# Performance work log

Hardware: AMD Instinct MI355X
Metric: run time of the kernel (lower is better)

## Reference

```python
import jax, jax.numpy as jnp
import numpy as np

N, D, R, B, K = 16384, 300, 10, 1024, 64


def setup_inputs() -> dict:
    key = jax.random.key(0)
    ks = jax.random.split(key, 6)
    return {
        "node_feat_src": jax.random.normal(ks[0], (N, D), jnp.float32),
        "node_feat_tgt": jax.random.normal(ks[1], (N, D), jnp.float32),
        "srcs_index": jax.random.randint(ks[2], (B, K), 0, N),
        "tgts_index": jax.random.randint(ks[3], (B, K), 0, N),
        "src_vs": jax.random.normal(ks[4], (R, D), jnp.float32),
        "tgt_vs": jax.random.normal(ks[5], (R, D), jnp.float32),
    }


def _tower(h, vs):
    # Householder chain: h @ (I - v v^T / (v^T v)) == h - ((h v) / (v^T v)) v^T
    def step(h, v):
        coef = (h @ v) / (v @ v)  # [N]
        return h - coef[:, None] * v[None, :], None
    h, _ = jax.lax.scan(step, h, vs)
    return h


def _l2norm(x):
    # matches F.normalize(p=2, eps=1e-12) over the last dim
    n = jnp.linalg.norm(x, axis=-1, keepdims=True)
    return x / jnp.maximum(n, 1e-12)


def reference(node_feat_src, node_feat_tgt, srcs_index, tgts_index, src_vs, tgt_vs):
    src_h = _tower(node_feat_src, src_vs)  # [N, D]
    tgt_h = _tower(node_feat_tgt, tgt_vs)  # [N, D]

    pos_src = _l2norm(src_h[srcs_index[:, 0]])  # [B, D]
    pos_tgt = _l2norm(tgt_h[tgts_index[:, 0]])  # [B, D]
    src_list = _l2norm(src_h[srcs_index])       # [B, K, D]
    tgt_list = _l2norm(tgt_h[tgts_index])       # [B, K, D]

    sim_src2tgt = jnp.einsum('bd,bkd->bk', pos_src, tgt_list)  # [B, K]
    sim_tgt2src = jnp.einsum('bd,bkd->bk', pos_tgt, src_list)  # [B, K]

    # CSLS hubness penalties: mean of top-10 cross-domain cosine sims
    sim_matrix = _l2norm(src_h) @ _l2norm(tgt_h).T  # [N, N]
    rt = jnp.mean(jax.lax.top_k(sim_matrix, 10)[0], axis=1)    # [N]
    rs = jnp.mean(jax.lax.top_k(sim_matrix.T, 10)[0], axis=1)  # [N]

    srcs_rt = rt[srcs_index]  # [B, K]
    tgts_rs = rs[tgts_index]  # [B, K]

    logits_src2tgt = sim_src2tgt * 2 - srcs_rt[:, 0:1] - tgts_rs
    logits_tgt2src = sim_tgt2src * 2 - tgts_rs[:, 0:1] - srcs_rt
    return logits_src2tgt, logits_tgt2src
```

## Files before the change

kernel.cpp:

```cpp
#include <hip/hip_runtime.h>
#include <hip/hip_bf16.h>

#define NN 16384
#define DD 300
#define DP 320
#define RR 10
#define BB 1024
#define KK 64
#define CAP 128
#define CAPL 512

typedef __attribute__((ext_vector_type(8))) short s8v;
typedef __attribute__((ext_vector_type(4))) float f4v;
typedef _Float16 h2 __attribute__((ext_vector_type(2)));

__device__ __forceinline__ unsigned mono2(unsigned d) {
    unsigned s = ((d >> 15) & 0x10001u) * 0xFFFFu;
    return d ^ (s | 0x80008000u);
}
__device__ __forceinline__ float key2f16(unsigned k) {
    unsigned short b = (k & 0x8000u) ? (unsigned short)(k ^ 0x8000u)
                                     : (unsigned short)(~k & 0xFFFFu);
    _Float16 hv = __builtin_bit_cast(_Float16, b);
    return (float)hv;
}

__device__ __forceinline__ h2 h2max(h2 a, h2 b) {
    return __builtin_elementwise_max(a, b);
}
__device__ __forceinline__ h2 hmax2s(h2 a, int xb) {
    int x = __shfl_xor(__builtin_bit_cast(int, a), xb);
    return h2max(a, __builtin_bit_cast(h2, x));
}
__device__ __forceinline__ h2 packh2(float a, float b) {
    h2 r; r[0] = (_Float16)a; r[1] = (_Float16)b; return r;
}

__device__ __forceinline__ void ins10(unsigned (&lst)[10], unsigned v) {
    #pragma unroll
    for (int q = 0; q < 10; ++q) {
        unsigned a  = lst[q];
        unsigned mx = a > v ? a : v;
        v           = a > v ? v : a;
        lst[q] = mx;
    }
}
__device__ __forceinline__ void ins10f(float (&lst)[10], float v) {
    #pragma unroll
    for (int q = 0; q < 10; ++q) {
        float a  = lst[q];
        float mx = fmaxf(a, v);
        v        = fminf(a, v);
        lst[q] = mx;
    }
}

__device__ __forceinline__ void xcd_map(int bid, int& by, int& bx) {
    const int xcd = bid & 7;
    const int s   = bid >> 3;
    bx = (xcd << 2) | (s & 3);
    by = s >> 2;
}

__device__ __forceinline__ void gload_lds16(const void* g, void* l) {
#if __has_builtin(__builtin_amdgcn_global_load_lds)
    __builtin_amdgcn_global_load_lds(
        (const __attribute__((address_space(1))) void*)g,
        (__attribute__((address_space(3))) void*)l, 16, 0, 0);
#else
    const int lane = threadIdx.x & 63;
    int4 v = *reinterpret_cast<const int4*>(g);
    *reinterpret_cast<int4*>((char*)l + lane * 16) = v;
#endif
}

__device__ __forceinline__ void stage_tile(
        const __hip_bfloat16* __restrict__ Ab, const __hip_bfloat16* __restrict__ Bb,
        int kb, char* base, int w, int lane) {
    const int r8 = lane >> 3;
    const int u  = (lane & 7) ^ r8;
    const int row = w * 8 + r8;
    const size_t go = (size_t)row * DP + kb * 64 + u * 8;
    gload_lds16(Ab + go, base + w * 1024);
    gload_lds16(Bb + go, base + 16384 + w * 1024);
}

__global__ __launch_bounds__(256) void tower_kernel(
        const float* __restrict__ feat, const float* __restrict__ vs,
        __hip_bfloat16* __restrict__ out) {
    __shared__ float vsh[RR * DD];
    const int tid = threadIdx.x;
    for (int i = tid; i < RR * DD; i += 256) vsh[i] = vs[i];
    __syncthreads();

    const int lane = tid & 63;
    const int wave = tid >> 6;
    const int row  = blockIdx.x * 4 + wave;

    float h[5];
    #pragma unroll
    for (int j = 0; j < 5; ++j) {
        int d = lane + 64 * j;
        h[j] = (d < DD) ? feat[(size_t)row * DD + d] : 0.f;
    }
    #pragma unroll
    for (int r = 0; r < RR; ++r) {
        float vl[5];
        float hv = 0.f, vv = 0.f;
        #pragma unroll
        for (int j = 0; j < 5; ++j) {
            int d = lane + 64 * j;
            float v = (d < DD) ? vsh[r * DD + d] : 0.f;
            vl[j] = v;
            hv += h[j] * v;
            vv += v * v;
        }
        #pragma unroll
        for (int o = 32; o; o >>= 1) {
            hv += __shfl_xor(hv, o);
            vv += __shfl_xor(vv, o);
        }
        float coef = hv / vv;
        #pragma unroll
        for (int j = 0; j < 5; ++j) h[j] -= coef * vl[j];
    }
    float nn = 0.f;
    #pragma unroll
    for (int j = 0; j < 5; ++j) nn += h[j] * h[j];
    #pragma unroll
    for (int o = 32; o; o >>= 1) nn += __shfl_xor(nn, o);
    float scale = 1.f / fmaxf(sqrtf(nn), 1e-12f);
    #pragma unroll
    for (int j = 0; j < 5; ++j) {
        int d = lane + 64 * j;
        float val = (d < DD) ? h[j] * scale : 0.f;
        out[(size_t)row * DP + d] = __float2bfloat16(val);
    }
}

#define KLOOP(COMPUTE_BODY)                                                    \
    stage_tile(Ab, Bb, 0, u_lds, w, lane);                                     \
    _Pragma("unroll")                                                          \
    for (int kb = 0; kb < 5; ++kb) {                                           \
        char* curb = u_lds + (kb & 1) * 32768;                                 \
        if (kb < 4)                                                            \
            stage_tile(Ab, Bb, kb + 1, u_lds + ((kb + 1) & 1) * 32768, w, lane); \
        if (kb < 4) { asm volatile("s_waitcnt vmcnt(2)" ::: "memory"); }       \
        else        { asm volatile("s_waitcnt vmcnt(0)" ::: "memory"); }       \
        __builtin_amdgcn_s_barrier();                                          \
        asm volatile("" ::: "memory");                                         \
        {                                                                      \
            const __hip_bfloat16* Asub = (const __hip_bfloat16*)curb;          \
            const __hip_bfloat16* Bsub = (const __hip_bfloat16*)(curb + 16384);\
            COMPUTE_BODY                                                       \
        }                                                                      \
        asm volatile("" ::: "memory");                                         \
        __builtin_amdgcn_s_barrier();                                          \
    }

#define COMPUTE_TILE                                                           \
    _Pragma("unroll")                                                          \
    for (int ks = 0; ks < 2; ++ks) {                                           \
        s8v af[2], bfv[2];                                                     \
        const int ulog = ks * 4 + (lane >> 4);                                 \
        const int up   = ulog ^ (lane & 7);                                    \
        _Pragma("unroll")                                                      \
        for (int m = 0; m < 2; ++m) {                                          \
            const int row = wr * 32 + m * 16 + (lane & 15);                    \
            af[m] = *reinterpret_cast<const s8v*>(Asub + row * 64 + up * 8);   \
        }                                                                      \
        _Pragma("unroll")                                                      \
        for (int n = 0; n < 2; ++n) {                                          \
            const int row = wc * 32 + n * 16 + (lane & 15);                    \
            bfv[n] = *reinterpret_cast<const s8v*>(Bsub + row * 64 + up * 8);  \
        }                                                                      \
        _Pragma("unroll")                                                      \
        for (int m = 0; m < 2; ++m)                                            \
            _Pragma("unroll")                                                  \
            for (int n = 0; n < 2; ++n)                                        \
                acc[m][n] = __builtin_amdgcn_mfma_f32_16x16x32_bf16(           \
                    af[m], bfv[n], acc[m][n], 0, 0, 0);                        \
    }

__global__ __launch_bounds__(1024) void passA_kernel(
        const __hip_bfloat16* __restrict__ A, const __hip_bfloat16* __restrict__ Bm,
        unsigned short* __restrict__ rowsmax_g,
        unsigned short* __restrict__ colsmax_g) {
    __shared__ __align__(16) char u_lds[65536];
    __shared__ unsigned short rowsm[16][512];
    __shared__ unsigned short colsm[512][16];

    const int tid = threadIdx.x;
    const int lane = tid & 63;
    const int w = tid >> 6;
    const int wr = w >> 2, wc = w & 3;
    int by, bx; xcd_map(blockIdx.x, by, bx);
    const int i0 = by * 512, j0 = bx * 512;

    for (int ti = 0; ti < 4; ++ti) {
        for (int tj = 0; tj < 4; ++tj) {
            f4v acc[2][2];
            #pragma unroll
            for (int m = 0; m < 2; ++m)
                #pragma unroll
                for (int n = 0; n < 2; ++n)
                    acc[m][n] = (f4v){0.f, 0.f, 0.f, 0.f};

            const __hip_bfloat16* Ab = A  + (size_t)(i0 + ti * 128) * DP;
            const __hip_bfloat16* Bb = Bm + (size_t)(j0 + tj * 128) * DP;

            KLOOP(COMPUTE_TILE)

            #pragma unroll
            for (int m = 0; m < 2; ++m) {
                h2 a01 = h2max(packh2(acc[m][0][0], acc[m][0][1]),
                               packh2(acc[m][1][0], acc[m][1][1]));
                h2 a23 = h2max(packh2(acc[m][0][2], acc[m][0][3]),
                               packh2(acc[m][1][2], acc[m][1][3]));
                a01 = hmax2s(a01, 1); a23 = hmax2s(a23, 1);
                a01 = hmax2s(a01, 2); a23 = hmax2s(a23, 2);
                a01 = hmax2s(a01, 4); a23 = hmax2s(a23, 4);
                a01 = hmax2s(a01, 8); a23 = hmax2s(a23, 8);
                if ((lane & 15) == m * 8) {
                    const int rl = ti * 128 + wr * 32 + m * 16 + ((lane >> 4) << 2);
                    uint2 u = make_uint2(mono2(__builtin_bit_cast(unsigned, a01)),
                                         mono2(__builtin_bit_cast(unsigned, a23)));
                    *reinterpret_cast<uint2*>(&rowsm[tj * 4 + wc][rl]) = u;
                }
            }
            {
                float rm0 = -1e30f, rm1 = -1e30f;
                #pragma unroll
                for (int m = 0; m < 2; ++m) {
                    rm0 = fmaxf(rm0, fmaxf(fmaxf(acc[m][0][0], acc[m][0][1]),
                                           fmaxf(acc[m][0][2], acc[m][0][3])));
                    rm1 = fmaxf(rm1, fmaxf(fmaxf(acc[m][1][0], acc[m][1][1]),
                                           fmaxf(acc[m][1][2], acc[m][1][3])));
                }
                h2 c = packh2(rm0, rm1);
                c = hmax2s(c, 16);
                c = hmax2s(c, 32);
                if ((lane >> 4) == 0) {
                    const int s = ti * 4 + wr;
                    const int cb = tj * 128 + wc * 32 + (lane & 15);
                    unsigned k = mono2(__builtin_bit_cast(unsigned, c));
                    colsm[cb][s]      = (unsigned short)(k & 0xFFFFu);
                    colsm[cb + 16][s] = (unsigned short)(k >> 16);
                }
            }
        }
    }
    __syncthreads();
    if (tid < 512) {
        const int r = tid;
        unsigned short t16[16];
        #pragma unroll
        for (int s = 0; s < 16; ++s) t16[s] = rowsm[s][r];
        uint4 o0, o1;
        o0.x = t16[0] | ((unsigned)t16[1] << 16);  o0.y = t16[2] | ((unsigned)t16[3] << 16);
        o0.z = t16[4] | ((unsigned)t16[5] << 16);  o0.w = t16[6] | ((unsigned)t16[7] << 16);
        o1.x = t16[8] | ((unsigned)t16[9] << 16);  o1.y = t16[10] | ((unsigned)t16[11] << 16);
        o1.z = t16[12] | ((unsigned)t16[13] << 16); o1.w = t16[14] | ((unsigned)t16[15] << 16);
        uint4* rdst = reinterpret_cast<uint4*>(rowsmax_g + (size_t)(i0 + r) * 512 + bx * 16);
        rdst[0] = o0; rdst[1] = o1;
    } else {
        const int r = tid - 512;
        uint4 q0 = *reinterpret_cast<uint4*>(&colsm[r][0]);
        uint4 q1 = *reinterpret_cast<uint4*>(&colsm[r][8]);
        uint4* cdst = reinterpret_cast<uint4*>(colsmax_g + (size_t)(j0 + r) * 512 + by * 16);
        cdst[0] = q0; cdst[1] = q1;
    }
}

__global__ __launch_bounds__(256) void thresh_kernel(
        const unsigned short* __restrict__ rowsmax_g,
        const unsigned short* __restrict__ colsmax_g,
        float* __restrict__ Tlb_row, float* __restrict__ Tlb_col,
        unsigned* __restrict__ rowcnt, unsigned* __restrict__ colcnt) {
    const int t = blockIdx.x * 256 + threadIdx.x;
    const bool isRow = t < NN;
    const int idx = isRow ? t : t - NN;
    const unsigned short* src = (isRow ? rowsmax_g : colsmax_g) + (size_t)idx * 512;

    unsigned lst[10];
    #pragma unroll
    for (int q = 0; q < 10; ++q) lst[q] = 0u;

    const uint4* p = reinterpret_cast<const uint4*>(src);
    for (int c = 0; c < 64; ++c) {
        uint4 q = p[c];
        unsigned v0 = q.x & 0xFFFFu, v1 = q.x >> 16;
        unsigned v2 = q.y & 0xFFFFu, v3 = q.y >> 16;
        unsigned v4 = q.z & 0xFFFFu, v5 = q.z >> 16;
        unsigned v6 = q.w & 0xFFFFu, v7 = q.w >> 16;
        unsigned g01 = v0 > v1 ? v0 : v1, g23 = v2 > v3 ? v2 : v3;
        unsigned g45 = v4 > v5 ? v4 : v5, g67 = v6 > v7 ? v6 : v7;
        unsigned ga = g01 > g23 ? g01 : g23, gb = g45 > g67 ? g45 : g67;
        unsigned g = ga > gb ? ga : gb;
        if (g > lst[9]) {
            if (v0 > lst[9]) ins10(lst, v0);
            if (v1 > lst[9]) ins10(lst, v1);
            if (v2 > lst[9]) ins10(lst, v2);
            if (v3 > lst[9]) ins10(lst, v3);
            if (v4 > lst[9]) ins10(lst, v4);
            if (v5 > lst[9]) ins10(lst, v5);
            if (v6 > lst[9]) ins10(lst, v6);
            if (v7 > lst[9]) ins10(lst, v7);
        }
    }
    float f = key2f16(lst[9]);
    float lb = f - fabsf(f) * 0.002f - 1e-6f;
    if (isRow) { Tlb_row[idx] = lb; rowcnt[idx] = 0u; }
    else       { Tlb_col[idx] = lb; colcnt[idx] = 0u; }
}

__global__ __launch_bounds__(1024) void passB_kernel(
        const __hip_bfloat16* __restrict__ A, const __hip_bfloat16* __restrict__ Bm,
        const float* __restrict__ Tlb_row, const float* __restrict__ Tlb_col,
        unsigned* __restrict__ rowcnt, unsigned* __restrict__ colcnt,
        float* __restrict__ rowbuf, float* __restrict__ colbuf) {
    __shared__ __align__(16) char u_lds[65536];
    __shared__ float Trow_s[512];
    __shared__ float Tcol_s[512];
    __shared__ unsigned scnt[2];
    __shared__ uint2 sbuf[2][CAPL];

    const int tid = threadIdx.x;
    const int lane = tid & 63;
    const int w = tid >> 6;
    const int wr = w >> 2, wc = w & 3;
    int by, bx; xcd_map(blockIdx.x, by, bx);
    const int i0 = by * 512, j0 = bx * 512;

    if (tid < 512) Trow_s[tid] = Tlb_row[i0 + tid];
    else           Tcol_s[tid - 512] = Tlb_col[j0 + tid - 512];
    if (tid < 2) scnt[tid] = 0u;
    __syncthreads();

    for (int ti = 0; ti < 4; ++ti) {
        float trmin = 1e30f;
        #pragma unroll
        for (int m = 0; m < 2; ++m)
            #pragma unroll
            for (int r = 0; r < 4; ++r)
                trmin = fminf(trmin, Trow_s[ti * 128 + wr * 32 + m * 16 + ((lane >> 4) << 2) + r]);

        for (int tj = 0; tj < 4; ++tj) {
            f4v acc[2][2];
            #pragma unroll
            for (int m = 0; m < 2; ++m)
                #pragma unroll
                for (int n = 0; n < 2; ++n)
                    acc[m][n] = (f4v){0.f, 0.f, 0.f, 0.f};

            const __hip_bfloat16* Ab = A  + (size_t)(i0 + ti * 128) * DP;
            const __hip_bfloat16* Bb = Bm + (size_t)(j0 + tj * 128) * DP;

            KLOOP(COMPUTE_TILE)

            const int c0i = tj * 128 + wc * 32 + (lane & 15);
            const int c1i = c0i + 16;
            const float tc0 = Tcol_s[c0i], tc1 = Tcol_s[c1i];
            float vm = -1e30f;
            #pragma unroll
            for (int m = 0; m < 2; ++m) {
                float a = fmaxf(fmaxf(acc[m][0][0], acc[m][0][1]),
                                fmaxf(acc[m][0][2], acc[m][0][3]));
                float b = fmaxf(fmaxf(acc[m][1][0], acc[m][1][1]),
                                fmaxf(acc[m][1][2], acc[m][1][3]));
                vm = fmaxf(vm, fmaxf(a, b));
            }
            if (vm >= fminf(trmin, fminf(tc0, tc1))) {
                #pragma unroll
                for (int m = 0; m < 2; ++m) {
                    #pragma unroll
                    for (int r = 0; r < 4; ++r) {
                        const int rl = ti * 128 + wr * 32 + m * 16 + ((lane >> 4) << 2) + r;
                        const float T = Trow_s[rl];
                        const float v0 = acc[m][0][r], v1 = acc[m][1][r];
                        if (v0 >= T) {
                            unsigned p = atomicAdd(&scnt[0], 1u);
                            if (p < CAPL) sbuf[0][p] = make_uint2((unsigned)(i0 + rl), __float_as_uint(v0));
                            else { unsigned q = atomicAdd(&rowcnt[i0 + rl], 1u);
                                   if (q < CAP) rowbuf[(size_t)(i0 + rl) * CAP + q] = v0; }
                        }
                        if (v1 >= T) {
                            unsigned p = atomicAdd(&scnt[0], 1u);
                            if (p < CAPL) sbuf[0][p] = make_uint2((unsigned)(i0 + rl), __float_as_uint(v1));
                            else { unsigned q = atomicAdd(&rowcnt[i0 + rl], 1u);
                                   if (q < CAP) rowbuf[(size_t)(i0 + rl) * CAP + q] = v1; }
                        }
                        if (v0 >= tc0) {
                            unsigned p = atomicAdd(&scnt[1], 1u);
                            if (p < CAPL) sbuf[1][p] = make_uint2((unsigned)(j0 + c0i), __float_as_uint(v0));
                            else { unsigned q = atomicAdd(&colcnt[j0 + c0i], 1u);
                                   if (q < CAP) colbuf[(size_t)(j0 + c0i) * CAP + q] = v0; }
                        }
                        if (v1 >= tc1) {
                            unsigned p = atomicAdd(&scnt[1], 1u);
                            if (p < CAPL) sbuf[1][p] = make_uint2((unsigned)(j0 + c1i), __float_as_uint(v1));
                            else { unsigned q = atomicAdd(&colcnt[j0 + c1i], 1u);
                                   if (q < CAP) colbuf[(size_t)(j0 + c1i) * CAP + q] = v1; }
                        }
                    }
                }
            }
        }
    }

    __syncthreads();
    {
        const unsigned nr = scnt[0] < CAPL ? scnt[0] : CAPL;
        const unsigned nc = scnt[1] < CAPL ? scnt[1] : CAPL;
        for (unsigned i = tid; i < nr; i += 1024) {
            uint2 e = sbuf[0][i];
            unsigned p = atomicAdd(&rowcnt[e.x], 1u);
            if (p < CAP) rowbuf[(size_t)e.x * CAP + p] = __uint_as_float(e.y);
        }
        for (unsigned i = tid; i < nc; i += 1024) {
            uint2 e = sbuf[1][i];
            unsigned p = atomicAdd(&colcnt[e.x], 1u);
            if (p < CAP) colbuf[(size_t)e.x * CAP + p] = __uint_as_float(e.y);
        }
    }
}

__global__ __launch_bounds__(256) void final_kernel(
        const unsigned* __restrict__ rowcnt, const unsigned* __restrict__ colcnt,
        const float* __restrict__ rowbuf, const float* __restrict__ colbuf,
        float* __restrict__ rt, float* __restrict__ rs) {
    const int t = blockIdx.x * 256 + threadIdx.x;
    const bool isRow = t < NN;
    const int idx = isRow ? t : t - NN;
    const unsigned cn = (isRow ? rowcnt : colcnt)[idx];
    const int n = (int)(cn < CAP ? cn : CAP);
    const float* buf = (isRow ? rowbuf : colbuf) + (size_t)idx * CAP;

    float lst[10];
    #pragma unroll
    for (int q = 0; q < 10; ++q) lst[q] = -1e30f;
    for (int i = 0; i < n; ++i) {
        float v = buf[i];
        if (v > lst[9]) ins10f(lst, v);
    }
    float s = 0.f;
    #pragma unroll
    for (int q = 0; q < 10; ++q) s += lst[q];
    s *= 0.1f;
    (isRow ? rt : rs)[idx] = s;
}

__global__ __launch_bounds__(256) void logits_kernel(
        const __hip_bfloat16* __restrict__ srcH, const __hip_bfloat16* __restrict__ tgtH,
        const int* __restrict__ sidx, const int* __restrict__ tidx,
        const float* __restrict__ rt, const float* __restrict__ rs,
        float* __restrict__ out) {
    const int b    = blockIdx.x;
    const int lane = threadIdx.x & 63;
    const int w    = threadIdx.x >> 6;

    const int s0 = sidx[b * KK];
    const int t0 = tidx[b * KK];
    float ps[5], pt[5];
    #pragma unroll
    for (int j = 0; j < 5; ++j) {
        int d = lane + 64 * j;
        ps[j] = __bfloat162float(srcH[(size_t)s0 * DP + d]);
        pt[j] = __bfloat162float(tgtH[(size_t)t0 * DP + d]);
    }
    const float rt_s0 = rt[s0];
    const float rs_t0 = rs[t0];

    for (int kk = w; kk < KK; kk += 4) {
        const int it = tidx[b * KK + kk];
        const int is = sidx[b * KK + kk];
        float a = 0.f, c = 0.f;
        #pragma unroll
        for (int j = 0; j < 5; ++j) {
            int d = lane + 64 * j;
            a += ps[j] * __bfloat162float(tgtH[(size_t)it * DP + d]);
            c += pt[j] * __bfloat162float(srcH[(size_t)is * DP + d]);
        }
        #pragma unroll
        for (int o = 32; o; o >>= 1) {
            a += __shfl_xor(a, o);
            c += __shfl_xor(c, o);
        }
        if (lane == 0) {
            out[b * KK + kk]           = 2.f * a - rt_s0 - rs[it];
            out[BB * KK + b * KK + kk] = 2.f * c - rs_t0 - rt[is];
        }
    }
}

extern "C" void kernel_launch(void* const* d_in, const int* in_sizes, int n_in,
                              void* d_out, int out_size, void* d_ws, size_t ws_size,
                              hipStream_t stream) {
    const float* nf_src = (const float*)d_in[0];
    const float* nf_tgt = (const float*)d_in[1];
    const int*   sidx   = (const int*)d_in[2];
    const int*   tidx   = (const int*)d_in[3];
    const float* svs    = (const float*)d_in[4];
    const float* tvs    = (const float*)d_in[5];

    char* ws = (char*)d_ws;
    const size_t SZ_H  = (size_t)NN * DP * 2;
    const size_t SZ_SM = (size_t)NN * 512 * 2;
    __hip_bfloat16* srcH = (__hip_bfloat16*)ws;
    __hip_bfloat16* tgtH = (__hip_bfloat16*)(ws + SZ_H);
    unsigned short* rowsmax = (unsigned short*)(ws + 2 * SZ_H);
    unsigned short* colsmax = (unsigned short*)(ws + 2 * SZ_H + SZ_SM);
    float* rowbuf = (float*)(ws + 2 * SZ_H);
    float* colbuf = (float*)(ws + 2 * SZ_H + (size_t)NN * CAP * 4);
    char* tail = ws + 2 * SZ_H + 2 * SZ_SM;
    float* Tlb_row = (float*)(tail);
    float* Tlb_col = (float*)(tail + 65536);
    unsigned* rowcnt = (unsigned*)(tail + 2 * 65536);
    unsigned* colcnt = (unsigned*)(tail + 3 * 65536);
    float* rt = (float*)(tail + 4 * 65536);
    float* rs = (float*)(tail + 5 * 65536);

    tower_kernel<<<NN / 4, 256, 0, stream>>>(nf_src, svs, srcH);
    tower_kernel<<<NN / 4, 256, 0, stream>>>(nf_tgt, tvs, tgtH);
    passA_kernel<<<1024, 1024, 0, stream>>>(srcH, tgtH, rowsmax, colsmax);
    thresh_kernel<<<(2 * NN) / 256, 256, 0, stream>>>(rowsmax, colsmax, Tlb_row, Tlb_col,
                                                      rowcnt, colcnt);
    passB_kernel<<<1024, 1024, 0, stream>>>(srcH, tgtH, Tlb_row, Tlb_col,
                                            rowcnt, colcnt, rowbuf, colbuf);
    final_kernel<<<(2 * NN) / 256, 256, 0, stream>>>(rowcnt, colcnt, rowbuf, colbuf, rt, rs);
    logits_kernel<<<BB, 256, 0, stream>>>(srcH, tgtH, sidx, tidx, rt, rs, (float*)d_out);
}
```

Baseline: 632.8 us.

## Use 256-thread blocks with 64x64 per-wave MFMA tiles in GEMM passes

Both GEMM passes now run 4 waves per block instead of 16, and each wave computes a 64x64 sub-tile (4x4 MFMA accumulators) instead of 32x32. This raises register-level reuse of the LDS fragments and cuts LDS read traffic per MFMA. In exchange the double-buffered async prefetch is replaced by a single buffer with syncthreads around each stage, so global loads no longer overlap compute inside a block. The max-reduction and threshold-scan epilogues are reworked to match the new accumulator layout.

```diff
diff --git a/kernel.cpp b/kernel.cpp
--- a/kernel.cpp
+++ b/kernel.cpp
@@ -34,6 +34,9 @@
 }
 __device__ __forceinline__ h2 packh2(float a, float b) {
     h2 r; r[0] = (_Float16)a; r[1] = (_Float16)b; return r;
+}
+__device__ __forceinline__ float max4(f4v v) {
+    return fmaxf(fmaxf(v[0], v[1]), fmaxf(v[2], v[3]));
 }
 
 __device__ __forceinline__ void ins10(unsigned (&lst)[10], unsigned v) {
@@ -79,10 +82,15 @@
         int kb, char* base, int w, int lane) {
     const int r8 = lane >> 3;
     const int u  = (lane & 7) ^ r8;
-    const int row = w * 8 + r8;
-    const size_t go = (size_t)row * DP + kb * 64 + u * 8;
-    gload_lds16(Ab + go, base + w * 1024);
-    gload_lds16(Bb + go, base + 16384 + w * 1024);
+    #pragma unroll
+    for (int qq = 0; qq < 8; ++qq) {
+        const int chunk = qq * 4 + w;
+        const int cm = chunk & 15;
+        const int row = cm * 8 + r8;
+        const size_t go = (size_t)row * DP + kb * 64 + u * 8;
+        gload_lds16((chunk < 16 ? Ab : Bb) + go,
+                    base + (chunk < 16 ? 0 : 16384) + cm * 1024);
+    }
 }
 
 __global__ __launch_bounds__(256) void tower_kernel(
@@ -138,121 +146,110 @@
     }
 }
 
-#define KLOOP(COMPUTE_BODY)                                                    \
-    stage_tile(Ab, Bb, 0, u_lds, w, lane);                                     \
+#define KLOOP64                                                                \
     _Pragma("unroll")                                                          \
     for (int kb = 0; kb < 5; ++kb) {                                           \
-        char* curb = u_lds + (kb & 1) * 32768;                                 \
-        if (kb < 4)                                                            \
-            stage_tile(Ab, Bb, kb + 1, u_lds + ((kb + 1) & 1) * 32768, w, lane); \
-        if (kb < 4) { asm volatile("s_waitcnt vmcnt(2)" ::: "memory"); }       \
-        else        { asm volatile("s_waitcnt vmcnt(0)" ::: "memory"); }       \
-        __builtin_amdgcn_s_barrier();                                          \
-        asm volatile("" ::: "memory");                                         \
-        {                                                                      \
-            const __hip_bfloat16* Asub = (const __hip_bfloat16*)curb;          \
-            const __hip_bfloat16* Bsub = (const __hip_bfloat16*)(curb + 16384);\
-            COMPUTE_BODY                                                       \
+        __syncthreads();                                                       \
+        stage_tile(Ab, Bb, kb, u_lds, w, lane);                                \
+        __syncthreads();                                                       \
+        _Pragma("unroll")                                                      \
+        for (int ks = 0; ks < 2; ++ks) {                                       \
+            s8v af[4], bfv[4];                                                 \
+            const int ulog = ks * 4 + (lane >> 4);                             \
+            const int up   = ulog ^ (lane & 7);                                \
+            _Pragma("unroll")                                                  \
+            for (int m = 0; m < 4; ++m) {                                      \
+                const int row = wr * 64 + m * 16 + (lane & 15);                \
+                af[m] = *reinterpret_cast<const s8v*>(Asub + row * 64 + up * 8); \
+            }                                                                  \
+            _Pragma("unroll")                                                  \
+            for (int n = 0; n < 4; ++n) {                                      \
+                const int row = wc * 64 + n * 16 + (lane & 15);                \
+                bfv[n] = *reinterpret_cast<const s8v*>(Bsub + row * 64 + up * 8); \
+            }                                                                  \
+            _Pragma("unroll")                                                  \
+            for (int m = 0; m < 4; ++m)                                        \
+                _Pragma("unroll")                                              \
+                for (int n = 0; n < 4; ++n)                                    \
+                    acc[m][n] = __builtin_amdgcn_mfma_f32_16x16x32_bf16(       \
+                        af[m], bfv[n], acc[m][n], 0, 0, 0);                    \
         }                                                                      \
-        asm volatile("" ::: "memory");                                         \
-        __builtin_amdgcn_s_barrier();                                          \
-    }
-
-#define COMPUTE_TILE                                                           \
-    _Pragma("unroll")                                                          \
-    for (int ks = 0; ks < 2; ++ks) {                                           \
-        s8v af[2], bfv[2];                                                     \
-        const int ulog = ks * 4 + (lane >> 4);                                 \
-        const int up   = ulog ^ (lane & 7);                                    \
-        _Pragma("unroll")                                                      \
-        for (int m = 0; m < 2; ++m) {                                          \
-            const int row = wr * 32 + m * 16 + (lane & 15);                    \
-            af[m] = *reinterpret_cast<const s8v*>(Asub + row * 64 + up * 8);   \
-        }                                                                      \
-        _Pragma("unroll")                                                      \
-        for (int n = 0; n < 2; ++n) {                                          \
-            const int row = wc * 32 + n * 16 + (lane & 15);                    \
-            bfv[n] = *reinterpret_cast<const s8v*>(Bsub + row * 64 + up * 8);  \
-        }                                                                      \
-        _Pragma("unroll")                                                      \
-        for (int m = 0; m < 2; ++m)                                            \
-            _Pragma("unroll")                                                  \
-            for (int n = 0; n < 2; ++n)                                        \
-                acc[m][n] = __builtin_amdgcn_mfma_f32_16x16x32_bf16(           \
-                    af[m], bfv[n], acc[m][n], 0, 0, 0);                        \
-    }
-
-__global__ __launch_bounds__(1024) void passA_kernel(
+    }
+
+__global__ __launch_bounds__(256) void passA_kernel(
         const __hip_bfloat16* __restrict__ A, const __hip_bfloat16* __restrict__ Bm,
         unsigned short* __restrict__ rowsmax_g,
         unsigned short* __restrict__ colsmax_g) {
-    __shared__ __align__(16) char u_lds[65536];
+    __shared__ __align__(16) char u_lds[32768];
     __shared__ unsigned short rowsm[16][512];
     __shared__ unsigned short colsm[512][16];
+
+    const __hip_bfloat16* Asub = (const __hip_bfloat16*)u_lds;
+    const __hip_bfloat16* Bsub = (const __hip_bfloat16*)(u_lds + 16384);
 
     const int tid = threadIdx.x;
     const int lane = tid & 63;
     const int w = tid >> 6;
-    const int wr = w >> 2, wc = w & 3;
+    const int wr = w >> 1, wc = w & 1;
     int by, bx; xcd_map(blockIdx.x, by, bx);
     const int i0 = by * 512, j0 = bx * 512;
 
     for (int ti = 0; ti < 4; ++ti) {
         for (int tj = 0; tj < 4; ++tj) {
-            f4v acc[2][2];
-            #pragma unroll
-            for (int m = 0; m < 2; ++m)
+            f4v acc[4][4];
+            #pragma unroll
+            for (int m = 0; m < 4; ++m)
                 #pragma unroll
-                for (int n = 0; n < 2; ++n)
+                for (int n = 0; n < 4; ++n)
                     acc[m][n] = (f4v){0.f, 0.f, 0.f, 0.f};
 
             const __hip_bfloat16* Ab = A  + (size_t)(i0 + ti * 128) * DP;
             const __hip_bfloat16* Bb = Bm + (size_t)(j0 + tj * 128) * DP;
 
-            KLOOP(COMPUTE_TILE)
-
-            #pragma unroll
-            for (int m = 0; m < 2; ++m) {
-                h2 a01 = h2max(packh2(acc[m][0][0], acc[m][0][1]),
-                               packh2(acc[m][1][0], acc[m][1][1]));
-                h2 a23 = h2max(packh2(acc[m][0][2], acc[m][0][3]),
-                               packh2(acc[m][1][2], acc[m][1][3]));
-                a01 = hmax2s(a01, 1); a23 = hmax2s(a23, 1);
-                a01 = hmax2s(a01, 2); a23 = hmax2s(a23, 2);
-                a01 = hmax2s(a01, 4); a23 = hmax2s(a23, 4);
-                a01 = hmax2s(a01, 8); a23 = hmax2s(a23, 8);
-                if ((lane & 15) == m * 8) {
-                    const int rl = ti * 128 + wr * 32 + m * 16 + ((lane >> 4) << 2);
-                    uint2 u = make_uint2(mono2(__builtin_bit_cast(unsigned, a01)),
-                                         mono2(__builtin_bit_cast(unsigned, a23)));
-                    *reinterpret_cast<uint2*>(&rowsm[tj * 4 + wc][rl]) = u;
+            KLOOP64
+
+            #pragma unroll
+            for (int p = 0; p < 2; ++p) {
+                #pragma unroll
+                for (int m = 0; m < 4; ++m) {
+                    h2 a01 = h2max(packh2(acc[m][2*p][0],   acc[m][2*p][1]),
+                                   packh2(acc[m][2*p+1][0], acc[m][2*p+1][1]));
+                    h2 a23 = h2max(packh2(acc[m][2*p][2],   acc[m][2*p][3]),
+                                   packh2(acc[m][2*p+1][2], acc[m][2*p+1][3]));
+                    a01 = hmax2s(a01, 1); a23 = hmax2s(a23, 1);
+                    a01 = hmax2s(a01, 2); a23 = hmax2s(a23, 2);
+                    a01 = hmax2s(a01, 4); a23 = hmax2s(a23, 4);
+                    a01 = hmax2s(a01, 8); a23 = hmax2s(a23, 8);
+                    if ((lane & 15) == m * 4) {
+                        const int rl = ti * 128 + wr * 64 + m * 16 + ((lane >> 4) << 2);
+                        uint2 u = make_uint2(mono2(__builtin_bit_cast(unsigned, a01)),
+                                             mono2(__builtin_bit_cast(unsigned, a23)));
+                        *reinterpret_cast<uint2*>(&rowsm[tj * 4 + wc * 2 + p][rl]) = u;
+                    }
                 }
             }
-            {
-                float rm0 = -1e30f, rm1 = -1e30f;
+            #pragma unroll
+            for (int q = 0; q < 2; ++q) {
                 #pragma unroll
-                for (int m = 0; m < 2; ++m) {
-                    rm0 = fmaxf(rm0, fmaxf(fmaxf(acc[m][0][0], acc[m][0][1]),
-                                           fmaxf(acc[m][0][2], acc[m][0][3])));
-                    rm1 = fmaxf(rm1, fmaxf(fmaxf(acc[m][1][0], acc[m][1][1]),
-                                           fmaxf(acc[m][1][2], acc[m][1][3])));
-                }
-                h2 c = packh2(rm0, rm1);
-                c = hmax2s(c, 16);
-                c = hmax2s(c, 32);
-                if ((lane >> 4) == 0) {
-                    const int s = ti * 4 + wr;
-                    const int cb = tj * 128 + wc * 32 + (lane & 15);
-                    unsigned k = mono2(__builtin_bit_cast(unsigned, c));
-                    colsm[cb][s]      = (unsigned short)(k & 0xFFFFu);
-                    colsm[cb + 16][s] = (unsigned short)(k >> 16);
+                for (int pr = 0; pr < 2; ++pr) {
+                    float ra = fmaxf(max4(acc[2*q][2*pr]),   max4(acc[2*q+1][2*pr]));
+                    float rb = fmaxf(max4(acc[2*q][2*pr+1]), max4(acc[2*q+1][2*pr+1]));
+                    h2 c = packh2(ra, rb);
+                    c = hmax2s(c, 16);
+                    c = hmax2s(c, 32);
+                    if ((lane >> 4) == 0) {
+                        const int s = ti * 4 + wr * 2 + q;
+                        const int cb = tj * 128 + wc * 64 + pr * 32 + (lane & 15);
+                        unsigned k = mono2(__builtin_bit_cast(unsigned, c));
+                        colsm[cb][s]      = (unsigned short)(k & 0xFFFFu);
+                        colsm[cb + 16][s] = (unsigned short)(k >> 16);
+                    }
                 }
             }
         }
     }
     __syncthreads();
-    if (tid < 512) {
-        const int r = tid;
+    for (int r = tid; r < 512; r += 256) {
         unsigned short t16[16];
         #pragma unroll
         for (int s = 0; s < 16; ++s) t16[s] = rowsm[s][r];
@@ -263,8 +260,8 @@
         o1.z = t16[12] | ((unsigned)t16[13] << 16); o1.w = t16[14] | ((unsigned)t16[15] << 16);
         uint4* rdst = reinterpret_cast<uint4*>(rowsmax_g + (size_t)(i0 + r) * 512 + bx * 16);
         rdst[0] = o0; rdst[1] = o1;
-    } else {
-        const int r = tid - 512;
+    }
+    for (int r = tid; r < 512; r += 256) {
         uint4 q0 = *reinterpret_cast<uint4*>(&colsm[r][0]);
         uint4 q1 = *reinterpret_cast<uint4*>(&colsm[r][8]);
         uint4* cdst = reinterpret_cast<uint4*>(colsmax_g + (size_t)(j0 + r) * 512 + by * 16);
@@ -314,93 +311,89 @@
     else       { Tlb_col[idx] = lb; colcnt[idx] = 0u; }
 }
 
-__global__ __launch_bounds__(1024) void passB_kernel(
+__global__ __launch_bounds__(256) void passB_kernel(
         const __hip_bfloat16* __restrict__ A, const __hip_bfloat16* __restrict__ Bm,
         const float* __restrict__ Tlb_row, const float* __restrict__ Tlb_col,
         unsigned* __restrict__ rowcnt, unsigned* __restrict__ colcnt,
         float* __restrict__ rowbuf, float* __restrict__ colbuf) {
-    __shared__ __align__(16) char u_lds[65536];
+    __shared__ __align__(16) char u_lds[32768];
     __shared__ float Trow_s[512];
     __shared__ float Tcol_s[512];
     __shared__ unsigned scnt[2];
     __shared__ uint2 sbuf[2][CAPL];
 
+    const __hip_bfloat16* Asub = (const __hip_bfloat16*)u_lds;
+    const __hip_bfloat16* Bsub = (const __hip_bfloat16*)(u_lds + 16384);
+
     const int tid = threadIdx.x;
     const int lane = tid & 63;
     const int w = tid >> 6;
-    const int wr = w >> 2, wc = w & 3;
+    const int wr = w >> 1, wc = w & 1;
     int by, bx; xcd_map(blockIdx.x, by, bx);
     const int i0 = by * 512, j0 = bx * 512;
 
-    if (tid < 512) Trow_s[tid] = Tlb_row[i0 + tid];
-    else           Tcol_s[tid - 512] = Tlb_col[j0 + tid - 512];
+    for (int i = tid; i < 512; i += 256) {
+        Trow_s[i] = Tlb_row[i0 + i];
+        Tcol_s[i] = Tlb_col[j0 + i];
+    }
     if (tid < 2) scnt[tid] = 0u;
     __syncthreads();
 
     for (int ti = 0; ti < 4; ++ti) {
         float trmin = 1e30f;
         #pragma unroll
-        for (int m = 0; m < 2; ++m)
+        for (int m = 0; m < 4; ++m)
             #pragma unroll
             for (int r = 0; r < 4; ++r)
-                trmin = fminf(trmin, Trow_s[ti * 128 + wr * 32 + m * 16 + ((lane >> 4) << 2) + r]);
+                trmin = fminf(trmin, Trow_s[ti * 128 + wr * 64 + m * 16 + ((lane >> 4) << 2) + r]);
 
         for (int tj = 0; tj < 4; ++tj) {
-            f4v acc[2][2];
-            #pragma unroll
-            for (int m = 0; m < 2; ++m)
+            f4v acc[4][4];
+            #pragma unroll
+            for (int m = 0; m < 4; ++m)
                 #pragma unroll
-                for (int n = 0; n < 2; ++n)
+                for (int n = 0; n < 4; ++n)
                     acc[m][n] = (f4v){0.f, 0.f, 0.f, 0.f};
 
             const __hip_bfloat16* Ab = A  + (size_t)(i0 + ti * 128) * DP;
             const __hip_bfloat16* Bb = Bm + (size_t)(j0 + tj * 128) * DP;
 
-            KLOOP(COMPUTE_TILE)
-
-            const int c0i = tj * 128 + wc * 32 + (lane & 15);
-            const int c1i = c0i + 16;
-            const float tc0 = Tcol_s[c0i], tc1 = Tcol_s[c1i];
+            KLOOP64
+
+            float tc[4];
+            #pragma unroll
+            for (int n = 0; n < 4; ++n)
+                tc[n] = Tcol_s[tj * 128 + wc * 64 + n * 16 + (lane & 15)];
+            float tcmin = fminf(fminf(tc[0], tc[1]), fminf(tc[2], tc[3]));
             float vm = -1e30f;
             #pragma unroll
-            for (int m = 0; m < 2; ++m) {
-                float a = fmaxf(fmaxf(acc[m][0][0], acc[m][0][1]),
-                                fmaxf(acc[m][0][2], acc[m][0][3]));
-                float b = fmaxf(fmaxf(acc[m][1][0], acc[m][1][1]),
-                                fmaxf(acc[m][1][2], acc[m][1][3]));
-                vm = fmaxf(vm, fmaxf(a, b));
-            }
-            if (vm >= fminf(trmin, fminf(tc0, tc1))) {
+            for (int m = 0; m < 4; ++m)
                 #pragma unroll
-                for (int m = 0; m < 2; ++m) {
+                for (int n = 0; n < 4; ++n)
+                    vm = fmaxf(vm, max4(acc[m][n]));
+            if (vm >= fminf(trmin, tcmin)) {
+                #pragma unroll
+                for (int m = 0; m < 4; ++m) {
                     #pragma unroll
                     for (int r = 0; r < 4; ++r) {
-                        const int rl = ti * 128 + wr * 32 + m * 16 + ((lane >> 4) << 2) + r;
+                        const int rl = ti * 128 + wr * 64 + m * 16 + ((lane >> 4) << 2) + r;
                         const float T = Trow_s[rl];
-                        const float v0 = acc[m][0][r], v1 = acc[m][1][r];
-                        if (v0 >= T) {
-                            unsigned p = atomicAdd(&scnt[0], 1u);
-                            if (p < CAPL) sbuf[0][p] = make_uint2((unsigned)(i0 + rl), __float_as_uint(v0));
-                            else { unsigned q = atomicAdd(&rowcnt[i0 + rl], 1u);
-                                   if (q < CAP) rowbuf[(size_t)(i0 + rl) * CAP + q] = v0; }
-                        }
-                        if (v1 >= T) {
-                            unsigned p = atomicAdd(&scnt[0], 1u);
-                            if (p < CAPL) sbuf[0][p] = make_uint2((unsigned)(i0 + rl), __float_as_uint(v1));
-                            else { unsigned q = atomicAdd(&rowcnt[i0 + rl], 1u);
-                                   if (q < CAP) rowbuf[(size_t)(i0 + rl) * CAP + q] = v1; }
-                        }
-                        if (v0 >= tc0) {
-                            unsigned p = atomicAdd(&scnt[1], 1u);
-                            if (p < CAPL) sbuf[1][p] = make_uint2((unsigned)(j0 + c0i), __float_as_uint(v0));
-                            else { unsigned q = atomicAdd(&colcnt[j0 + c0i], 1u);
-                                   if (q < CAP) colbuf[(size_t)(j0 + c0i) * CAP + q] = v0; }
-                        }
-                        if (v1 >= tc1) {
-                            unsigned p = atomicAdd(&scnt[1], 1u);
-                            if (p < CAPL) sbuf[1][p] = make_uint2((unsigned)(j0 + c1i), __float_as_uint(v1));
-                            else { unsigned q = atomicAdd(&colcnt[j0 + c1i], 1u);
-                                   if (q < CAP) colbuf[(size_t)(j0 + c1i) * CAP + q] = v1; }
+                        #pragma unroll
+                        for (int n = 0; n < 4; ++n) {
+                            const float v = acc[m][n][r];
+                            if (v >= T) {
+                                unsigned p = atomicAdd(&scnt[0], 1u);
+                                if (p < CAPL) sbuf[0][p] = make_uint2((unsigned)(i0 + rl), __float_as_uint(v));
+                                else { unsigned qq = atomicAdd(&rowcnt[i0 + rl], 1u);
+                                       if (qq < CAP) rowbuf[(size_t)(i0 + rl) * CAP + qq] = v; }
+                            }
+                            if (v >= tc[n]) {
+                                const int cn = j0 + tj * 128 + wc * 64 + n * 16 + (lane & 15);
+                                unsigned p = atomicAdd(&scnt[1], 1u);
+                                if (p < CAPL) sbuf[1][p] = make_uint2((unsigned)cn, __float_as_uint(v));
+                                else { unsigned qq = atomicAdd(&colcnt[cn], 1u);
+                                       if (qq < CAP) colbuf[(size_t)cn * CAP + qq] = v; }
+                            }
                         }
                     }
                 }
@@ -412,12 +405,12 @@
     {
         const unsigned nr = scnt[0] < CAPL ? scnt[0] : CAPL;
         const unsigned nc = scnt[1] < CAPL ? scnt[1] : CAPL;
-        for (unsigned i = tid; i < nr; i += 1024) {
+        for (unsigned i = tid; i < nr; i += 256) {
             uint2 e = sbuf[0][i];
             unsigned p = atomicAdd(&rowcnt[e.x], 1u);
             if (p < CAP) rowbuf[(size_t)e.x * CAP + p] = __uint_as_float(e.y);
         }
-        for (unsigned i = tid; i < nc; i += 1024) {
+        for (unsigned i = tid; i < nc; i += 256) {
             uint2 e = sbuf[1][i];
             unsigned p = atomicAdd(&colcnt[e.x], 1u);
             if (p < CAP) colbuf[(size_t)e.x * CAP + p] = __uint_as_float(e.y);
@@ -522,11 +515,11 @@
 
     tower_kernel<<<NN / 4, 256, 0, stream>>>(nf_src, svs, srcH);
     tower_kernel<<<NN / 4, 256, 0, stream>>>(nf_tgt, tvs, tgtH);
-    passA_kernel<<<1024, 1024, 0, stream>>>(srcH, tgtH, rowsmax, colsmax);
+    passA_kernel<<<1024, 256, 0, stream>>>(srcH, tgtH, rowsmax, colsmax);
     thresh_kernel<<<(2 * NN) / 256, 256, 0, stream>>>(rowsmax, colsmax, Tlb_row, Tlb_col,
                                                       rowcnt, colcnt);
-    passB_kernel<<<1024, 1024, 0, stream>>>(srcH, tgtH, Tlb_row, Tlb_col,
-                                            rowcnt, colcnt, rowbuf, colbuf);
+    passB_kernel<<<1024, 256, 0, stream>>>(srcH, tgtH, Tlb_row, Tlb_col,
+                                           rowcnt, colcnt, rowbuf, colbuf);
     final_kernel<<<(2 * NN) / 256, 256, 0, stream>>>(rowcnt, colcnt, rowbuf, colbuf, rt, rs);
     logits_kernel<<<BB, 256, 0, stream>>>(srcH, tgtH, sidx, tidx, rt, rs, (float*)d_out);
 }
```

Result: slower. 881.4 us (+39.3%).

## Flatten tile loops into triple-buffered pipeline prefetching across output tiles

Applied to the files above, without the earlier changes.

Replaces the per-tile double-buffered K loop with a flattened loop over all 16 output tiles of the block, using three LDS stages. Loads run two k-blocks ahead, continue into the first k-blocks of the next tile, and drop one barrier per k step. The aim is to hide the prologue load latency at each tile start and cut synchronisation overhead. In exchange LDS use grows from 64 KB to 96 KB per block, and the vmcnt wait counts must be exactly right to stay correct.

```diff
diff --git a/kernel.cpp b/kernel.cpp
--- a/kernel.cpp
+++ b/kernel.cpp
@@ -137,26 +137,6 @@
         out[(size_t)row * DP + d] = __float2bfloat16(val);
     }
 }
-
-#define KLOOP(COMPUTE_BODY)                                                    \
-    stage_tile(Ab, Bb, 0, u_lds, w, lane);                                     \
-    _Pragma("unroll")                                                          \
-    for (int kb = 0; kb < 5; ++kb) {                                           \
-        char* curb = u_lds + (kb & 1) * 32768;                                 \
-        if (kb < 4)                                                            \
-            stage_tile(Ab, Bb, kb + 1, u_lds + ((kb + 1) & 1) * 32768, w, lane); \
-        if (kb < 4) { asm volatile("s_waitcnt vmcnt(2)" ::: "memory"); }       \
-        else        { asm volatile("s_waitcnt vmcnt(0)" ::: "memory"); }       \
-        __builtin_amdgcn_s_barrier();                                          \
-        asm volatile("" ::: "memory");                                         \
-        {                                                                      \
-            const __hip_bfloat16* Asub = (const __hip_bfloat16*)curb;          \
-            const __hip_bfloat16* Bsub = (const __hip_bfloat16*)(curb + 16384);\
-            COMPUTE_BODY                                                       \
-        }                                                                      \
-        asm volatile("" ::: "memory");                                         \
-        __builtin_amdgcn_s_barrier();                                          \
-    }
 
 #define COMPUTE_TILE                                                           \
     _Pragma("unroll")                                                          \
@@ -182,11 +162,36 @@
                     af[m], bfv[n], acc[m][n], 0, 0, 0);                        \
     }
 
+#define KLOOP_FLAT                                                             \
+    _Pragma("unroll")                                                          \
+    for (int kb = 0; kb < 5; ++kb) {                                           \
+        __builtin_amdgcn_s_barrier();                                          \
+        if (kb < 3) {                                                          \
+            stage_tile(Ab, Bb, kb + 2,                                         \
+                       u_lds + ((2 * t + kb + 2) % 3) * 32768, w, lane);       \
+        } else if (t < 15) {                                                   \
+            stage_tile(An, Bn, kb - 3,                                         \
+                       u_lds + ((2 * t + kb + 2) % 3) * 32768, w, lane);       \
+        }                                                                      \
+        if (t == 15 && kb == 3) { asm volatile("s_waitcnt vmcnt(2)" ::: "memory"); } \
+        else if (t == 15 && kb == 4) { asm volatile("s_waitcnt vmcnt(0)" ::: "memory"); } \
+        else { asm volatile("s_waitcnt vmcnt(4)" ::: "memory"); }              \
+        __builtin_amdgcn_s_barrier();                                          \
+        asm volatile("" ::: "memory");                                         \
+        {                                                                      \
+            const char* curb = u_lds + ((2 * t + kb) % 3) * 32768;             \
+            const __hip_bfloat16* Asub = (const __hip_bfloat16*)curb;          \
+            const __hip_bfloat16* Bsub = (const __hip_bfloat16*)(curb + 16384);\
+            COMPUTE_TILE                                                       \
+        }                                                                      \
+        asm volatile("" ::: "memory");                                         \
+    }
+
 __global__ __launch_bounds__(1024) void passA_kernel(
         const __hip_bfloat16* __restrict__ A, const __hip_bfloat16* __restrict__ Bm,
         unsigned short* __restrict__ rowsmax_g,
         unsigned short* __restrict__ colsmax_g) {
-    __shared__ __align__(16) char u_lds[65536];
+    __shared__ __align__(16) char u_lds[98304];
     __shared__ unsigned short rowsm[16][512];
     __shared__ unsigned short colsm[512][16];
 
@@ -197,56 +202,65 @@
     int by, bx; xcd_map(blockIdx.x, by, bx);
     const int i0 = by * 512, j0 = bx * 512;
 
-    for (int ti = 0; ti < 4; ++ti) {
-        for (int tj = 0; tj < 4; ++tj) {
-            f4v acc[2][2];
+    {
+        const __hip_bfloat16* A0 = A  + (size_t)i0 * DP;
+        const __hip_bfloat16* B0 = Bm + (size_t)j0 * DP;
+        stage_tile(A0, B0, 0, u_lds, w, lane);
+        stage_tile(A0, B0, 1, u_lds + 32768, w, lane);
+    }
+
+    for (int t = 0; t < 16; ++t) {
+        const int ti = t >> 2, tj = t & 3;
+        const __hip_bfloat16* Ab = A  + (size_t)(i0 + ti * 128) * DP;
+        const __hip_bfloat16* Bb = Bm + (size_t)(j0 + tj * 128) * DP;
+        const int tn = (t + 1) & 15;
+        const __hip_bfloat16* An = A  + (size_t)(i0 + (tn >> 2) * 128) * DP;
+        const __hip_bfloat16* Bn = Bm + (size_t)(j0 + (tn & 3) * 128) * DP;
+
+        f4v acc[2][2];
+        #pragma unroll
+        for (int m = 0; m < 2; ++m)
             #pragma unroll
-            for (int m = 0; m < 2; ++m)
-                #pragma unroll
-                for (int n = 0; n < 2; ++n)
-                    acc[m][n] = (f4v){0.f, 0.f, 0.f, 0.f};
-
-            const __hip_bfloat16* Ab = A  + (size_t)(i0 + ti * 128) * DP;
-            const __hip_bfloat16* Bb = Bm + (size_t)(j0 + tj * 128) * DP;
-
-            KLOOP(COMPUTE_TILE)
-
+            for (int n = 0; n < 2; ++n)
+                acc[m][n] = (f4v){0.f, 0.f, 0.f, 0.f};
+
+        KLOOP_FLAT
+
+        #pragma unroll
+        for (int m = 0; m < 2; ++m) {
+            h2 a01 = h2max(packh2(acc[m][0][0], acc[m][0][1]),
+                           packh2(acc[m][1][0], acc[m][1][1]));
+            h2 a23 = h2max(packh2(acc[m][0][2], acc[m][0][3]),
+                           packh2(acc[m][1][2], acc[m][1][3]));
+            a01 = hmax2s(a01, 1); a23 = hmax2s(a23, 1);
+            a01 = hmax2s(a01, 2); a23 = hmax2s(a23, 2);
+            a01 = hmax2s(a01, 4); a23 = hmax2s(a23, 4);
+            a01 = hmax2s(a01, 8); a23 = hmax2s(a23, 8);
+            if ((lane & 15) == m * 8) {
+                const int rl = ti * 128 + wr * 32 + m * 16 + ((lane >> 4) << 2);
+                uint2 u = make_uint2(mono2(__builtin_bit_cast(unsigned, a01)),
+                                     mono2(__builtin_bit_cast(unsigned, a23)));
+                *reinterpret_cast<uint2*>(&rowsm[tj * 4 + wc][rl]) = u;
+            }
+        }
+        {
+            float rm0 = -1e30f, rm1 = -1e30f;
             #pragma unroll
             for (int m = 0; m < 2; ++m) {
-                h2 a01 = h2max(packh2(acc[m][0][0], acc[m][0][1]),
-                               packh2(acc[m][1][0], acc[m][1][1]));
-                h2 a23 = h2max(packh2(acc[m][0][2], acc[m][0][3]),
-                               packh2(acc[m][1][2], acc[m][1][3]));
-                a01 = hmax2s(a01, 1); a23 = hmax2s(a23, 1);
-                a01 = hmax2s(a01, 2); a23 = hmax2s(a23, 2);
-                a01 = hmax2s(a01, 4); a23 = hmax2s(a23, 4);
-                a01 = hmax2s(a01, 8); a23 = hmax2s(a23, 8);
-                if ((lane & 15) == m * 8) {
-                    const int rl = ti * 128 + wr * 32 + m * 16 + ((lane >> 4) << 2);
-                    uint2 u = make_uint2(mono2(__builtin_bit_cast(unsigned, a01)),
-                                         mono2(__builtin_bit_cast(unsigned, a23)));
-                    *reinterpret_cast<uint2*>(&rowsm[tj * 4 + wc][rl]) = u;
-                }
+                rm0 = fmaxf(rm0, fmaxf(fmaxf(acc[m][0][0], acc[m][0][1]),
+                                       fmaxf(acc[m][0][2], acc[m][0][3])));
+                rm1 = fmaxf(rm1, fmaxf(fmaxf(acc[m][1][0], acc[m][1][1]),
+                                       fmaxf(acc[m][1][2], acc[m][1][3])));
             }
-            {
-                float rm0 = -1e30f, rm1 = -1e30f;
-                #pragma unroll
-                for (int m = 0; m < 2; ++m) {
-                    rm0 = fmaxf(rm0, fmaxf(fmaxf(acc[m][0][0], acc[m][0][1]),
-                                           fmaxf(acc[m][0][2], acc[m][0][3])));
-                    rm1 = fmaxf(rm1, fmaxf(fmaxf(acc[m][1][0], acc[m][1][1]),
-                                           fmaxf(acc[m][1][2], acc[m][1][3])));
-                }
-                h2 c = packh2(rm0, rm1);
-                c = hmax2s(c, 16);
-                c = hmax2s(c, 32);
-                if ((lane >> 4) == 0) {
-                    const int s = ti * 4 + wr;
-                    const int cb = tj * 128 + wc * 32 + (lane & 15);
-                    unsigned k = mono2(__builtin_bit_cast(unsigned, c));
-                    colsm[cb][s]      = (unsigned short)(k & 0xFFFFu);
-                    colsm[cb + 16][s] = (unsigned short)(k >> 16);
-                }
+            h2 c = packh2(rm0, rm1);
+            c = hmax2s(c, 16);
+            c = hmax2s(c, 32);
+            if ((lane >> 4) == 0) {
+                const int s = ti * 4 + wr;
+                const int cb = tj * 128 + wc * 32 + (lane & 15);
+                unsigned k = mono2(__builtin_bit_cast(unsigned, c));
+                colsm[cb][s]      = (unsigned short)(k & 0xFFFFu);
+                colsm[cb + 16][s] = (unsigned short)(k >> 16);
             }
         }
     }
@@ -319,7 +333,7 @@
         const float* __restrict__ Tlb_row, const float* __restrict__ Tlb_col,
         unsigned* __restrict__ rowcnt, unsigned* __restrict__ colcnt,
         float* __restrict__ rowbuf, float* __restrict__ colbuf) {
-    __shared__ __align__(16) char u_lds[65536];
+    __shared__ __align__(16) char u_lds[98304];
     __shared__ float Trow_s[512];
     __shared__ float Tcol_s[512];
     __shared__ unsigned scnt[2];
@@ -337,7 +351,21 @@
     if (tid < 2) scnt[tid] = 0u;
     __syncthreads();
 
-    for (int ti = 0; ti < 4; ++ti) {
+    {
+        const __hip_bfloat16* A0 = A  + (size_t)i0 * DP;
+        const __hip_bfloat16* B0 = Bm + (size_t)j0 * DP;
+        stage_tile(A0, B0, 0, u_lds, w, lane);
+        stage_tile(A0, B0, 1, u_lds + 32768, w, lane);
+    }
+
+    for (int t = 0; t < 16; ++t) {
+        const int ti = t >> 2, tj = t & 3;
+        const __hip_bfloat16* Ab = A  + (size_t)(i0 + ti * 128) * DP;
+        const __hip_bfloat16* Bb = Bm + (size_t)(j0 + tj * 128) * DP;
+        const int tn = (t + 1) & 15;
+        const __hip_bfloat16* An = A  + (size_t)(i0 + (tn >> 2) * 128) * DP;
+        const __hip_bfloat16* Bn = Bm + (size_t)(j0 + (tn & 3) * 128) * DP;
+
         float trmin = 1e30f;
         #pragma unroll
         for (int m = 0; m < 2; ++m)
@@ -345,63 +373,58 @@
             for (int r = 0; r < 4; ++r)
                 trmin = fminf(trmin, Trow_s[ti * 128 + wr * 32 + m * 16 + ((lane >> 4) << 2) + r]);
 
-        for (int tj = 0; tj < 4; ++tj) {
-            f4v acc[2][2];
+        f4v acc[2][2];
+        #pragma unroll
+        for (int m = 0; m < 2; ++m)
             #pragma unroll
-            for (int m = 0; m < 2; ++m)
-                #pragma unroll
-                for (int n = 0; n < 2; ++n)
-                    acc[m][n] = (f4v){0.f, 0.f, 0.f, 0.f};
-
-            const __hip_bfloat16* Ab = A  + (size_t)(i0 + ti * 128) * DP;
-            const __hip_bfloat16* Bb = Bm + (size_t)(j0 + tj * 128) * DP;
-
-            KLOOP(COMPUTE_TILE)
-
-            const int c0i = tj * 128 + wc * 32 + (lane & 15);
-            const int c1i = c0i + 16;
-            const float tc0 = Tcol_s[c0i], tc1 = Tcol_s[c1i];
-            float vm = -1e30f;
+            for (int n = 0; n < 2; ++n)
+                acc[m][n] = (f4v){0.f, 0.f, 0.f, 0.f};
+
+        KLOOP_FLAT
+
+        const int c0i = tj * 128 + wc * 32 + (lane & 15);
+        const int c1i = c0i + 16;
+        const float tc0 = Tcol_s[c0i], tc1 = Tcol_s[c1i];
+        float vm = -1e30f;
+        #pragma unroll
+        for (int m = 0; m < 2; ++m) {
+            float a = fmaxf(fmaxf(acc[m][0][0], acc[m][0][1]),
+                            fmaxf(acc[m][0][2], acc[m][0][3]));
+            float b = fmaxf(fmaxf(acc[m][1][0], acc[m][1][1]),
+                            fmaxf(acc[m][1][2], acc[m][1][3]));
+            vm = fmaxf(vm, fmaxf(a, b));
+        }
+        if (vm >= fminf(trmin, fminf(tc0, tc1))) {
             #pragma unroll
             for (int m = 0; m < 2; ++m) {
-                float a = fmaxf(fmaxf(acc[m][0][0], acc[m][0][1]),
-                                fmaxf(acc[m][0][2], acc[m][0][3]));
-                float b = fmaxf(fmaxf(acc[m][1][0], acc[m][1][1]),
-                                fmaxf(acc[m][1][2], acc[m][1][3]));
-                vm = fmaxf(vm, fmaxf(a, b));
-            }
-            if (vm >= fminf(trmin, fminf(tc0, tc1))) {
                 #pragma unroll
-                for (int m = 0; m < 2; ++m) {
-                    #pragma unroll
-                    for (int r = 0; r < 4; ++r) {
-                        const int rl = ti * 128 + wr * 32 + m * 16 + ((lane >> 4) << 2) + r;
-                        const float T = Trow_s[rl];
-                        const float v0 = acc[m][0][r], v1 = acc[m][1][r];
-                        if (v0 >= T) {
-                            unsigned p = atomicAdd(&scnt[0], 1u);
-                            if (p < CAPL) sbuf[0][p] = make_uint2((unsigned)(i0 + rl), __float_as_uint(v0));
-                            else { unsigned q = atomicAdd(&rowcnt[i0 + rl], 1u);
-                                   if (q < CAP) rowbuf[(size_t)(i0 + rl) * CAP + q] = v0; }
-                        }
-                        if (v1 >= T) {
-                            unsigned p = atomicAdd(&scnt[0], 1u);
-                            if (p < CAPL) sbuf[0][p] = make_uint2((unsigned)(i0 + rl), __float_as_uint(v1));
-                            else { unsigned q = atomicAdd(&rowcnt[i0 + rl], 1u);
-                                   if (q < CAP) rowbuf[(size_t)(i0 + rl) * CAP + q] = v1; }
-                        }
-                        if (v0 >= tc0) {
-                            unsigned p = atomicAdd(&scnt[1], 1u);
-                            if (p < CAPL) sbuf[1][p] = make_uint2((unsigned)(j0 + c0i), __float_as_uint(v0));
-                            else { unsigned q = atomicAdd(&colcnt[j0 + c0i], 1u);
-                                   if (q < CAP) colbuf[(size_t)(j0 + c0i) * CAP + q] = v0; }
-                        }
-                        if (v1 >= tc1) {
-                            unsigned p = atomicAdd(&scnt[1], 1u);
-                            if (p < CAPL) sbuf[1][p] = make_uint2((unsigned)(j0 + c1i), __float_as_uint(v1));
-                            else { unsigned q = atomicAdd(&colcnt[j0 + c1i], 1u);
-                                   if (q < CAP) colbuf[(size_t)(j0 + c1i) * CAP + q] = v1; }
-                        }
+                for (int r = 0; r < 4; ++r) {
+                    const int rl = ti * 128 + wr * 32 + m * 16 + ((lane >> 4) << 2) + r;
+                    const float T = Trow_s[rl];
+                    const float v0 = acc[m][0][r], v1 = acc[m][1][r];
+                    if (v0 >= T) {
+                        unsigned p = atomicAdd(&scnt[0], 1u);
+                        if (p < CAPL) sbuf[0][p] = make_uint2((unsigned)(i0 + rl), __float_as_uint(v0));
+                        else { unsigned q = atomicAdd(&rowcnt[i0 + rl], 1u);
+                               if (q < CAP) rowbuf[(size_t)(i0 + rl) * CAP + q] = v0; }
+                    }
+                    if (v1 >= T) {
+                        unsigned p = atomicAdd(&scnt[0], 1u);
+                        if (p < CAPL) sbuf[0][p] = make_uint2((unsigned)(i0 + rl), __float_as_uint(v1));
+                        else { unsigned q = atomicAdd(&rowcnt[i0 + rl], 1u);
+                               if (q < CAP) rowbuf[(size_t)(i0 + rl) * CAP + q] = v1; }
+                    }
+                    if (v0 >= tc0) {
+                        unsigned p = atomicAdd(&scnt[1], 1u);
+                        if (p < CAPL) sbuf[1][p] = make_uint2((unsigned)(j0 + c0i), __float_as_uint(v0));
+                        else { unsigned q = atomicAdd(&colcnt[j0 + c0i], 1u);
+                               if (q < CAP) colbuf[(size_t)(j0 + c0i) * CAP + q] = v0; }
+                    }
+                    if (v1 >= tc1) {
+                        unsigned p = atomicAdd(&scnt[1], 1u);
+                        if (p < CAPL) sbuf[1][p] = make_uint2((unsigned)(j0 + c1i), __float_as_uint(v1));
+                        else { unsigned q = atomicAdd(&colcnt[j0 + c1i], 1u);
+                               if (q < CAP) colbuf[(size_t)(j0 + c1i) * CAP + q] = v1; }
                     }
                 }
             }
```

Result: slower. 703.8 us (+11.2%).
